# Kernel tuning notes

Measured on AMD Instinct MI355X. Metric: run time of the kernel, lower is better.

The kernel has to match this reference:

```python
import jax, jax.numpy as jnp
import numpy as np

B, L, D_IN, D_MODEL, D_OUT, N_LAYERS, N2 = 16, 2048, 512, 512, 512, 4, 32
Q_STEP = 1.0 / 64.0
LN_EPS = 1e-5


def setup_inputs() -> dict:
    key = jax.random.key(0)
    ks = jax.random.split(key, 12)
    H = D_MODEL
    x = jax.random.normal(ks[0], (B, D_IN, L), jnp.float32)
    # sigma-delta dense encoder / decoder weights (ANN-equivalent: dense + ReLU)
    W_enc = jax.random.normal(ks[1], (H, D_IN), jnp.float32) * (1.0 / np.sqrt(D_IN))
    W_dec = jax.random.normal(ks[2], (D_OUT, H), jnp.float32) * (1.0 / np.sqrt(H))
    # S4D kernel params, stacked over layers. S4D-Lin init.
    log_dt = (jax.random.uniform(ks[3], (N_LAYERS, H), jnp.float32)
              * (np.log(0.1) - np.log(0.001)) + np.log(0.001))
    log_A_real = jnp.full((N_LAYERS, H, N2), np.log(0.5), jnp.float32)
    A_imag = jnp.tile((np.pi * jnp.arange(N2, dtype=jnp.float32))[None, None, :],
                      (N_LAYERS, H, 1))
    C_re = jax.random.normal(ks[4], (N_LAYERS, H, N2), jnp.float32) * (0.5 ** 0.5)
    C_im = jax.random.normal(ks[5], (N_LAYERS, H, N2), jnp.float32) * (0.5 ** 0.5)
    D = jax.random.normal(ks[6], (N_LAYERS, H), jnp.float32)
    # output linear of each S4D block: 1x1 conv H -> 2H followed by GLU
    W_out = jax.random.normal(ks[7], (N_LAYERS, 2 * H, H), jnp.float32) * (1.0 / np.sqrt(H))
    b_out = jnp.zeros((N_LAYERS, 2 * H), jnp.float32)
    ln_g = jnp.ones((N_LAYERS, H), jnp.float32)
    ln_b = jnp.zeros((N_LAYERS, H), jnp.float32)
    return {"x": x, "W_enc": W_enc, "W_dec": W_dec, "log_dt": log_dt,
            "log_A_real": log_A_real, "A_imag": A_imag, "C_re": C_re,
            "C_im": C_im, "D": D, "W_out": W_out, "b_out": b_out,
            "ln_g": ln_g, "ln_b": ln_b}


def _quantize_ste(x, step):
    q = jnp.round(x / step) * step
    return x + jax.lax.stop_gradient(q - x)


def reference(x, W_enc, W_dec, log_dt, log_A_real, A_imag, C_re, C_im, D,
              W_out, b_out, ln_g, ln_b):
    # x: (B, d_input, L) channel-time layout (slayer convention)
    xq = _quantize_ste(x, Q_STEP)
    h = jax.nn.relu(jnp.einsum('bct,dc->bdt', xq, W_enc))  # encoder (B,H,L)
    Lx = h.shape[-1]
    t = jnp.arange(Lx)
    for i in range(N_LAYERS):
        # ---- S4D kernel (ZOH-style discretization) ----
        dt = jnp.exp(log_dt[i])[:, None]                 # (H,1)
        A = -jnp.exp(log_A_real[i]) + 1j * A_imag[i]     # (H,N)
        dtA = dt * A                                     # (H,N)
        Cc = (C_re[i] + 1j * C_im[i]) * jnp.expm1(dtA) / A
        vand = jnp.exp(dtA[:, :, None] * t)              # (H,N,L)
        K = 2.0 * jnp.einsum('hn,hnl->hl', Cc, vand).real  # (H,L)
        # ---- FFT convolution ----
        k_f = jnp.fft.rfft(K, n=2 * Lx)                  # (H, L+1)
        u_f = jnp.fft.rfft(h, n=2 * Lx)                  # (B,H,L+1)
        y = jnp.fft.irfft(u_f * k_f[None], n=2 * Lx)[..., :Lx]
        y = y + D[i][:, None] * h                        # skip connection
        y = jax.nn.gelu(y, approximate=False)
        # output linear: 1x1 conv H->2H + GLU over channel dim
        z = jnp.einsum('bht,dh->bdt', y, W_out[i]) + b_out[i][None, :, None]
        z = z[:, :D_MODEL] * jax.nn.sigmoid(z[:, D_MODEL:])
        # residual + post-norm (LayerNorm over channel dim)
        h = z + h
        mu = h.mean(axis=1, keepdims=True)
        var = h.var(axis=1, keepdims=True)
        h = (h - mu) / jnp.sqrt(var + LN_EPS) * ln_g[i][:, None] + ln_b[i][:, None]
    out = jax.nn.relu(jnp.einsum('bht,dh->bdt', h, W_dec))  # decoder (B,d_out,L)
    return out
```

## Files before the change

kernel.cpp:

```cpp
#include <hip/hip_runtime.h>
#include <cstdint>
#include <cstddef>

typedef __attribute__((ext_vector_type(8))) short short8;
typedef __attribute__((ext_vector_type(8))) _Float16 half8;
typedef __attribute__((ext_vector_type(4))) float floatx4;
typedef __attribute__((ext_vector_type(4))) int intx4;
typedef __attribute__((ext_vector_type(4))) unsigned short ushort4v;

__device__ __forceinline__ unsigned short f2h(float f) {
    union { _Float16 h; unsigned short u; } v;
    v.h = (_Float16)f;
    return v.u;
}
__device__ __forceinline__ float h2f(unsigned short u) {
    union { unsigned short u; _Float16 h; } v;
    v.u = u;
    return (float)v.h;
}
__device__ __forceinline__ float relu_keepnan(float v) {
    return v > 0.f ? v : (v == v ? 0.f : v);
}

__global__ __launch_bounds__(256) void k_cvt(
    const float* __restrict__ src, unsigned short* __restrict__ dst, int n) {
    int i = blockIdx.x * 256 + threadIdx.x;
    if (i < n) dst[i] = f2h(src[i]);
}

__global__ __launch_bounds__(256) void k_precompute(
    const float* __restrict__ ldt, const float* __restrict__ lar,
    const float* __restrict__ aim, const float* __restrict__ cre,
    const float* __restrict__ cim, float4* __restrict__ lwc,
    float2* __restrict__ wt) {
    int idx = blockIdx.x * 256 + threadIdx.x;
    int i = idx >> 14;
    int h = (idx >> 5) & 511;
    int n = idx & 31;
    float dt = expf(ldt[i * 512 + h]);
    float Are = -expf(lar[idx]);
    float Aim = aim[idx];
    float dre = dt * Are, dim = dt * Aim;
    float e = expf(dre);
    float wre = e * cosf(dim);
    float wim = e * sinf(dim);
    float emr = wre - 1.f, emi = wim;
    float inv = 1.f / (Are * Are + Aim * Aim);
    float fr = (emr * Are + emi * Aim) * inv;
    float fi = (emi * Are - emr * Aim) * inv;
    float cr = cre[idx], ci = cim[idx];
    float4 o;
    o.x = wre; o.y = wim;
    o.z = 2.f * (cr * fr - ci * fi);
    o.w = 2.f * (cr * fi + ci * fr);
    int oidx = (i * 32 + n) * 512 + h;
    lwc[oidx] = o;
    float ar = wre, ai = wim;
#pragma unroll
    for (int k = 0; k < 7; ++k) {
        float nr = ar * ar - ai * ai;
        float ni = 2.f * ar * ai;
        ar = nr; ai = ni;
    }
    wt[oidx] = make_float2(ar, ai);
}

__global__ __launch_bounds__(256) void k_quant_transpose(
    const float* __restrict__ x, unsigned short* __restrict__ xq, int b0) {
    __shared__ unsigned short tile[64][65];
    const int bg = b0 + blockIdx.z, bl = blockIdx.z;
    const int c0 = blockIdx.y * 64, t0 = blockIdx.x * 64;
    const int tid = threadIdx.x;
#pragma unroll
    for (int it = 0; it < 16; ++it) {
        int idx = it * 256 + tid;
        int r = idx >> 6, cc = idx & 63;
        float f = x[(size_t)(bg * 512 + c0 + r) * 2048 + t0 + cc];
        float q = rintf(f * 64.f) * 0.015625f;
        tile[r][cc] = f2h(q);
    }
    __syncthreads();
#pragma unroll
    for (int it = 0; it < 16; ++it) {
        int idx = it * 256 + tid;
        int r = idx >> 6, cc = idx & 63;
        xq[(size_t)(bl * 2048 + t0 + r) * 512 + c0 + cc] = tile[cc][r];
    }
}

__global__ __launch_bounds__(64) void k_build_wa(
    const float4* __restrict__ lwc, unsigned short* __restrict__ WA, int layer) {
    __shared__ unsigned short Ws[64 * 136];
    const int h = blockIdx.x, tid = threadIdx.x;
    if (tid < 32) {
        float4 v = lwc[((size_t)layer * 32 + tid) * 512 + h];
        float pr = 1.f, pi = 0.f;
        for (int m = 0; m < 128; ++m) {
            Ws[(2 * tid) * 136 + (127 - m)] = f2h(pr);
            Ws[(2 * tid + 1) * 136 + (127 - m)] = f2h(pi);
            float nr = pr * v.x - pi * v.y;
            float ni = pr * v.y + pi * v.x;
            pr = nr; pi = ni;
        }
    }
    __syncthreads();
#pragma unroll
    for (int it = 0; it < 16; ++it) {
        int idx = it * 64 + tid;
        int r = idx >> 4, c8 = idx & 15;
        *(intx4*)(WA + (size_t)h * 8192 + r * 128 + c8 * 8) =
            *(const intx4*)(Ws + r * 136 + c8 * 8);
    }
}

__global__ __launch_bounds__(256) void k_build_T(
    const float4* __restrict__ lwc, const float* __restrict__ Dp,
    unsigned short* __restrict__ TT, int layer) {
    __shared__ float Kvs[128];
    __shared__ unsigned short Mxs[128 * 64];
    __shared__ float wr_s[32], wi_s[32], cr_s[32], ci_s[32];
    const int h = blockIdx.x, tid = threadIdx.x;
    if (tid < 32) {
        float4 v = lwc[((size_t)layer * 32 + tid) * 512 + h];
        wr_s[tid] = v.x; wi_s[tid] = v.y; cr_s[tid] = v.z; ci_s[tid] = v.w;
    }
    __syncthreads();
    if (tid < 32) {
        const int n = tid;
        float wre = wr_s[n], wim = wi_s[n];
        float ar = cr_s[n], ai = ci_s[n];
        for (int m = 0; m <= 128; ++m) {
            if (m < 128) {
                float s = ar;
#pragma unroll
                for (int d = 16; d >= 1; d >>= 1) s += __shfl_xor(s, d, 64);
                if (n == 0) Kvs[m] = s;
            }
            if (m >= 1) {
                Mxs[(m - 1) * 64 + 2 * n] = f2h(ar);
                Mxs[(m - 1) * 64 + 2 * n + 1] = f2h(-ai);
            }
            float nr = ar * wre - ai * wim;
            float ni = ar * wim + ai * wre;
            ar = nr; ai = ni;
        }
    }
    __syncthreads();
    const float Dh = Dp[layer * 512 + h];
#pragma unroll
    for (int it = 0; it < 12; ++it) {
        int idx = it * 256 + tid;
        int t = idx / 24, c8 = idx % 24;
        short8 pack;
#pragma unroll
        for (int q = 0; q < 8; ++q) {
            int k = c8 * 8 + q;
            unsigned short us;
            if (k < 128) {
                float val = (k <= t) ? (Kvs[t - k] + (k == t ? Dh : 0.f)) : 0.f;
                us = f2h(val);
            } else {
                us = Mxs[t * 64 + (k - 128)];
            }
            pack[q] = (short)us;
        }
        *(short8*)(TT + (size_t)h * 24576 + t * 192 + c8 * 8) = pack;
    }
}

template <int MODE>
__global__ __launch_bounds__(256, 2) void k_gemm(
    const unsigned short* __restrict__ A, const unsigned short* __restrict__ Bm,
    float* __restrict__ of32, unsigned short* __restrict__ o16,
    unsigned short* __restrict__ ut, int J, int b0) {
    __shared__ __align__(16) unsigned short lds[2 * 128 * 72];
    unsigned short* Al = lds;
    unsigned short* Bl = lds + 128 * 72;
    const int tid = threadIdx.x;
    const int m0 = blockIdx.y * 128;
    const int j0 = blockIdx.x * 128;
    const int sub = tid & 7;
    const int row = tid >> 3;
    const unsigned short* Ag = A + (size_t)(m0 + row) * 512 + sub * 8;
    const unsigned short* Bg = Bm + (size_t)(j0 + row) * 512 + sub * 8;
    intx4 ra[4], rb[4];
#pragma unroll
    for (int i = 0; i < 4; ++i) {
        ra[i] = *(const intx4*)(Ag + (size_t)i * 32 * 512);
        rb[i] = *(const intx4*)(Bg + (size_t)i * 32 * 512);
    }
    const int lane = tid & 63;
    const int w = tid >> 6;
    const int wm = w & 1, wn = w >> 1;
    const int l15 = lane & 15, quad = lane >> 4;
    floatx4 acc[4][4] = {};
    for (int kt = 0; kt < 8; ++kt) {
#pragma unroll
        for (int i = 0; i < 4; ++i) {
            *(intx4*)(Al + (row + 32 * i) * 72 + sub * 8) = ra[i];
            *(intx4*)(Bl + (row + 32 * i) * 72 + sub * 8) = rb[i];
        }
        __syncthreads();
        if (kt < 7) {
#pragma unroll
            for (int i = 0; i < 4; ++i) {
                ra[i] = *(const intx4*)(Ag + (size_t)i * 32 * 512 + (kt + 1) * 64);
                rb[i] = *(const intx4*)(Bg + (size_t)i * 32 * 512 + (kt + 1) * 64);
            }
        }
#pragma unroll
        for (int ks = 0; ks < 2; ++ks) {
            half8 af[4], bfr[4];
#pragma unroll
            for (int mt = 0; mt < 4; ++mt)
                af[mt] = *(const half8*)(Al + (wm * 64 + mt * 16 + l15) * 72 + ks * 32 + quad * 8);
#pragma unroll
            for (int nt = 0; nt < 4; ++nt)
                bfr[nt] = *(const half8*)(Bl + (wn * 64 + nt * 16 + l15) * 72 + ks * 32 + quad * 8);
#pragma unroll
            for (int mt = 0; mt < 4; ++mt)
#pragma unroll
                for (int nt = 0; nt < 4; ++nt)
                    acc[mt][nt] = __builtin_amdgcn_mfma_f32_16x16x32_f16(
                        af[mt], bfr[nt], acc[mt][nt], 0, 0, 0);
        }
        __syncthreads();
    }
#pragma unroll
    for (int mt = 0; mt < 4; ++mt) {
#pragma unroll
        for (int nt = 0; nt < 4; ++nt) {
            const int dl = wm * 64 + mt * 16 + quad * 4;
            const int jl = wn * 64 + nt * 16 + l15;
            floatx4 v = acc[mt][nt];
#pragma unroll
            for (int r = 0; r < 4; ++r) v[r] = relu_keepnan(v[r]);
            if (MODE == 0) {
                ushort4v hv;
#pragma unroll
                for (int r = 0; r < 4; ++r) hv[r] = f2h(v[r]);
                *(ushort4v*)(o16 + (size_t)(j0 + jl) * 512 + m0 + dl) = hv;
#pragma unroll
                for (int r = 0; r < 4; ++r) lds[(dl + r) * 136 + jl] = hv[r];
            } else {
                const int j = j0 + jl;
                const int bl = j >> 11, t = j & 2047;
#pragma unroll
                for (int r = 0; r < 4; ++r)
                    of32[((size_t)((b0 + bl) * 512 + m0 + dl + r)) * 2048 + t] = v[r];
            }
        }
    }
    if (MODE == 0) {
        __syncthreads();
        const int drow = tid >> 1, hh = tid & 1;
        const unsigned short* srcp = lds + drow * 136 + hh * 64;
        unsigned short* dstp = ut + (size_t)(m0 + drow) * J + j0 + hh * 64;
#pragma unroll
        for (int q = 0; q < 8; ++q)
            *(intx4*)(dstp + q * 8) = *(const intx4*)(srcp + q * 8);
    }
}

__global__ __launch_bounds__(256, 4) void k_stateA(
    const unsigned short* __restrict__ WA, const unsigned short* __restrict__ ut,
    float* __restrict__ P, int J, int Rtot) {
    __shared__ __align__(16) unsigned short Aw[64 * 72];
    __shared__ __align__(16) unsigned short Bw[128 * 72];
    const int tid = threadIdx.x;
    const int h = blockIdx.y;
    const int r0 = blockIdx.x * 128;
    const int sub = tid & 7, row = tid >> 3;
    const unsigned short* Ag = WA + (size_t)h * 8192 + row * 128 + sub * 8;
    const unsigned short* Bg = ut + (size_t)h * J + (size_t)(r0 + row) * 128 + sub * 8;
    intx4 ra[2], rb[4];
    ra[0] = *(const intx4*)(Ag);
    ra[1] = *(const intx4*)(Ag + 32 * 128);
#pragma unroll
    for (int i = 0; i < 4; ++i) rb[i] = *(const intx4*)(Bg + i * 32 * 128);
    const int lane = tid & 63, w = tid >> 6;
    const int wm = w & 1, wn = w >> 1;
    const int l15 = lane & 15, quad = lane >> 4;
    floatx4 acc[2][4] = {};
    for (int kt = 0; kt < 2; ++kt) {
        *(intx4*)(Aw + row * 72 + sub * 8) = ra[0];
        *(intx4*)(Aw + (row + 32) * 72 + sub * 8) = ra[1];
#pragma unroll
        for (int i = 0; i < 4; ++i)
            *(intx4*)(Bw + (row + 32 * i) * 72 + sub * 8) = rb[i];
        __syncthreads();
        if (kt == 0) {
            ra[0] = *(const intx4*)(Ag + 64);
            ra[1] = *(const intx4*)(Ag + 32 * 128 + 64);
#pragma unroll
            for (int i = 0; i < 4; ++i) rb[i] = *(const intx4*)(Bg + i * 32 * 128 + 64);
        }
#pragma unroll
        for (int ks = 0; ks < 2; ++ks) {
            half8 af[2], bfr[4];
#pragma unroll
            for (int mt = 0; mt < 2; ++mt)
                af[mt] = *(const half8*)(Aw + (wm * 32 + mt * 16 + l15) * 72 + ks * 32 + quad * 8);
#pragma unroll
            for (int nt = 0; nt < 4; ++nt)
                bfr[nt] = *(const half8*)(Bw + (wn * 64 + nt * 16 + l15) * 72 + ks * 32 + quad * 8);
#pragma unroll
            for (int mt = 0; mt < 2; ++mt)
#pragma unroll
                for (int nt = 0; nt < 4; ++nt)
                    acc[mt][nt] = __builtin_amdgcn_mfma_f32_16x16x32_f16(
                        af[mt], bfr[nt], acc[mt][nt], 0, 0, 0);
        }
        __syncthreads();
    }
#pragma unroll
    for (int mt = 0; mt < 2; ++mt)
#pragma unroll
        for (int nt = 0; nt < 4; ++nt)
#pragma unroll
            for (int r = 0; r < 4; ++r)
                P[((size_t)h * 64 + wm * 32 + mt * 16 + quad * 4 + r) * Rtot +
                  r0 + wn * 64 + nt * 16 + l15] = acc[mt][nt][r];
}

__global__ __launch_bounds__(64) void k_comb(
    const float* __restrict__ P, const float2* __restrict__ wt,
    unsigned short* __restrict__ S0, int layer, int Rtot) {
    __shared__ float Ps[64][17];
    __shared__ unsigned short S0s[16][64];
    const int h = blockIdx.x, bl = blockIdx.y;
    const int tid = threadIdx.x;
#pragma unroll
    for (int it = 0; it < 4; ++it) {
        int idx = it * 64 + tid;
        int n2 = idx >> 2, pt = idx & 3;
        float4 v = *(const float4*)(P + ((size_t)h * 64 + n2) * Rtot + bl * 16 + pt * 4);
        Ps[n2][pt * 4 + 0] = v.x; Ps[n2][pt * 4 + 1] = v.y;
        Ps[n2][pt * 4 + 2] = v.z; Ps[n2][pt * 4 + 3] = v.w;
    }
    __syncthreads();
    if (tid < 32) {
        const int n = tid;
        float2 wv = wt[((size_t)layer * 32 + n) * 512 + h];
        float ar = 0.f, ai = 0.f;
        for (int g = 0; g < 16; ++g) {
            S0s[g][2 * n] = f2h(ar);
            S0s[g][2 * n + 1] = f2h(ai);
            float pr = Ps[2 * n][g], pi = Ps[2 * n + 1][g];
            float nr = fmaf(wv.x, ar, fmaf(-wv.y, ai, pr));
            float ni = fmaf(wv.x, ai, fmaf(wv.y, ar, pi));
            ar = nr; ai = ni;
        }
    }
    __syncthreads();
    const int g = tid >> 2, pt = tid & 3;
    unsigned short* dst = S0 + ((size_t)h * Rtot + bl * 16 + g) * 64 + pt * 16;
    *(intx4*)(dst) = *(const intx4*)(&S0s[g][pt * 16]);
    *(intx4*)(dst + 8) = *(const intx4*)(&S0s[g][pt * 16 + 8]);
}

__global__ __launch_bounds__(256, 2) void k_applyB(
    const unsigned short* __restrict__ TT, const unsigned short* __restrict__ ut,
    const unsigned short* __restrict__ S0, unsigned short* __restrict__ vt,
    int J, int Rtot) {
    __shared__ __align__(16) unsigned short lds[2 * 128 * 72];
    unsigned short* Al = lds;
    unsigned short* Bl = lds + 128 * 72;
    const int tid = threadIdx.x;
    const int h = blockIdx.y;
    const int r0 = blockIdx.x * 128;
    const int sub = tid & 7, row = tid >> 3;
    const unsigned short* Ag = TT + (size_t)h * 24576 + row * 192 + sub * 8;
    const unsigned short* Bu = ut + (size_t)h * J + (size_t)(r0 + row) * 128 + sub * 8;
    const unsigned short* Bs = S0 + ((size_t)h * Rtot + r0 + row) * 64 + sub * 8;
    intx4 ra[4], rb[4];
#pragma unroll
    for (int i = 0; i < 4; ++i) {
        ra[i] = *(const intx4*)(Ag + i * 32 * 192);
        rb[i] = *(const intx4*)(Bu + i * 32 * 128);
    }
    const int lane = tid & 63, w = tid >> 6;
    const int wm = w & 1, wn = w >> 1;
    const int l15 = lane & 15, quad = lane >> 4;
    floatx4 acc[4][4] = {};
    for (int kt = 0; kt < 3; ++kt) {
#pragma unroll
        for (int i = 0; i < 4; ++i) {
            *(intx4*)(Al + (row + 32 * i) * 72 + sub * 8) = ra[i];
            *(intx4*)(Bl + (row + 32 * i) * 72 + sub * 8) = rb[i];
        }
        __syncthreads();
        if (kt == 0) {
#pragma unroll
            for (int i = 0; i < 4; ++i) {
                ra[i] = *(const intx4*)(Ag + i * 32 * 192 + 64);
                rb[i] = *(const intx4*)(Bu + i * 32 * 128 + 64);
            }
        } else if (kt == 1) {
#pragma unroll
            for (int i = 0; i < 4; ++i) {
                ra[i] = *(const intx4*)(Ag + i * 32 * 192 + 128);
                rb[i] = *(const intx4*)(Bs + i * 32 * 64);
            }
        }
#pragma unroll
        for (int ks = 0; ks < 2; ++ks) {
            half8 af[4], bfr[4];
#pragma unroll
            for (int mt = 0; mt < 4; ++mt)
                af[mt] = *(const half8*)(Al + (wm * 64 + mt * 16 + l15) * 72 + ks * 32 + quad * 8);
#pragma unroll
            for (int nt = 0; nt < 4; ++nt)
                bfr[nt] = *(const half8*)(Bl + (wn * 64 + nt * 16 + l15) * 72 + ks * 32 + quad * 8);
#pragma unroll
            for (int mt = 0; mt < 4; ++mt)
#pragma unroll
                for (int nt = 0; nt < 4; ++nt)
                    acc[mt][nt] = __builtin_amdgcn_mfma_f32_16x16x32_f16(
                        af[mt], bfr[nt], acc[mt][nt], 0, 0, 0);
        }
        __syncthreads();
    }
#pragma unroll
    for (int mt = 0; mt < 4; ++mt)
#pragma unroll
        for (int nt = 0; nt < 4; ++nt) {
            const int tl = wm * 64 + mt * 16 + quad * 4;
            const int rl = wn * 64 + nt * 16 + l15;
            ushort4v pack;
#pragma unroll
            for (int r = 0; r < 4; ++r) {
                float y = acc[mt][nt][r];
                float ge = 0.5f * y * (1.f + erff(y * 0.70710678118654752f));
                pack[r] = f2h(ge);
            }
            *(ushort4v*)(lds + rl * 136 + tl) = pack;
        }
    __syncthreads();
    const int rl2 = tid >> 1, hh = tid & 1;
    const unsigned short* srcp = lds + rl2 * 136 + hh * 64;
    unsigned short* dstp = vt + (size_t)h * J + (size_t)(r0 + rl2) * 128 + hh * 64;
#pragma unroll
    for (int q = 0; q < 8; ++q)
        *(intx4*)(dstp + q * 8) = *(const intx4*)(srcp + q * 8);
}

__global__ __launch_bounds__(256, 2) void k_gemm_glu(
    const unsigned short* __restrict__ A,
    const unsigned short* __restrict__ Bt,
    const float* __restrict__ bias,
    unsigned short* __restrict__ g_out, int J) {
    __shared__ __align__(16) unsigned short lds[3 * 128 * 72];
    unsigned short* A1l = lds;
    unsigned short* A2l = lds + 9216;
    unsigned short* Bl  = lds + 18432;
    const int tid = threadIdx.x;
    const int m0 = blockIdx.y * 128;
    const int j0 = blockIdx.x * 128;
    const int sub = tid & 7;
    const int row = tid >> 3;
    const unsigned short* A1g = A + (size_t)(m0 + row) * 512 + sub * 8;
    const unsigned short* A2g = A1g + 512 * 512;
    const int chp = tid >> 3, jo = tid & 7;
    const unsigned short* Bg = Bt + (size_t)(2 * chp) * J + j0 + jo * 8;
    intx4 ra1[4], ra2[4], rb[4];
#pragma unroll
    for (int i = 0; i < 4; ++i) {
        ra1[i] = *(const intx4*)(A1g + (size_t)i * 32 * 512);
        ra2[i] = *(const intx4*)(A2g + (size_t)i * 32 * 512);
    }
    rb[0] = *(const intx4*)(Bg);
    rb[1] = *(const intx4*)(Bg + J);
    rb[2] = *(const intx4*)(Bg + 64);
    rb[3] = *(const intx4*)(Bg + J + 64);
    const int lane = tid & 63;
    const int w = tid >> 6;
    const int wm = w & 1, wn = w >> 1;
    const int l15 = lane & 15, quad = lane >> 4;
    const int colbase = (((chp >> 2) ^ jo) << 3) + (chp & 3) * 2;
    floatx4 ac1[4][4] = {}, ac2[4][4] = {};
    for (int kt = 0; kt < 8; ++kt) {
#pragma unroll
        for (int i = 0; i < 4; ++i) {
            *(intx4*)(A1l + (row + 32 * i) * 72 + sub * 8) = ra1[i];
            *(intx4*)(A2l + (row + 32 * i) * 72 + sub * 8) = ra2[i];
        }
        {
            unsigned int* B32 = (unsigned int*)Bl;
#pragma unroll
            for (int half = 0; half < 2; ++half) {
                const int jb = (jo + half * 8) * 8;
                intx4 e0 = rb[half * 2], e1 = rb[half * 2 + 1];
#pragma unroll
                for (int i = 0; i < 4; ++i) {
                    unsigned int ae = (unsigned int)e0[i], be = (unsigned int)e1[i];
                    unsigned int lo = (ae & 0xffffu) | (be << 16);
                    unsigned int hi = (ae >> 16) | (be & 0xffff0000u);
                    B32[((jb + 2 * i) * 72 + colbase) >> 1] = lo;
                    B32[((jb + 2 * i + 1) * 72 + colbase) >> 1] = hi;
                }
            }
        }
        __syncthreads();
        if (kt < 7) {
#pragma unroll
            for (int i = 0; i < 4; ++i) {
                ra1[i] = *(const intx4*)(A1g + (size_t)i * 32 * 512 + (kt + 1) * 64);
                ra2[i] = *(const intx4*)(A2g + (size_t)i * 32 * 512 + (kt + 1) * 64);
            }
            rb[0] = *(const intx4*)(Bg + (size_t)(kt + 1) * 64 * J);
            rb[1] = *(const intx4*)(Bg + (size_t)(kt + 1) * 64 * J + J);
            rb[2] = *(const intx4*)(Bg + (size_t)(kt + 1) * 64 * J + 64);
            rb[3] = *(const intx4*)(Bg + (size_t)(kt + 1) * 64 * J + J + 64);
        }
#pragma unroll
        for (int ks = 0; ks < 2; ++ks) {
            half8 af1[4], af2[4], bfr[4];
#pragma unroll
            for (int mt = 0; mt < 4; ++mt) {
                af1[mt] = *(const half8*)(A1l + (wm * 64 + mt * 16 + l15) * 72 + ks * 32 + quad * 8);
                af2[mt] = *(const half8*)(A2l + (wm * 64 + mt * 16 + l15) * 72 + ks * 32 + quad * 8);
            }
#pragma unroll
            for (int nt = 0; nt < 4; ++nt) {
                const int rr = wn * 64 + nt * 16 + l15;
                const int cb = (ks * 4 + quad) ^ ((rr >> 3) & 7);
                bfr[nt] = *(const half8*)(Bl + rr * 72 + cb * 8);
            }
#pragma unroll
            for (int mt = 0; mt < 4; ++mt)
#pragma unroll
                for (int nt = 0; nt < 4; ++nt) {
                    ac1[mt][nt] = __builtin_amdgcn_mfma_f32_16x16x32_f16(
                        af1[mt], bfr[nt], ac1[mt][nt], 0, 0, 0);
                    ac2[mt][nt] = __builtin_amdgcn_mfma_f32_16x16x32_f16(
                        af2[mt], bfr[nt], ac2[mt][nt], 0, 0, 0);
                }
        }
        __syncthreads();
    }
#pragma unroll
    for (int mt = 0; mt < 4; ++mt) {
#pragma unroll
        for (int nt = 0; nt < 4; ++nt) {
            const int dl = wm * 64 + mt * 16 + quad * 4;
            const int jl = wn * 64 + nt * 16 + l15;
            ushort4v p;
#pragma unroll
            for (int r = 0; r < 4; ++r) {
                float a = ac1[mt][nt][r] + bias[m0 + dl + r];
                float gg = ac2[mt][nt][r] + bias[512 + m0 + dl + r];
                p[r] = f2h(a / (1.f + expf(-gg)));
            }
            *(ushort4v*)(lds + jl * 136 + dl) = p;
        }
    }
    __syncthreads();
    const int r2 = tid >> 1, hh = tid & 1;
    const unsigned short* srcp = lds + r2 * 136 + hh * 64;
    unsigned short* dstp = g_out + (size_t)(j0 + r2) * 512 + m0 + hh * 64;
#pragma unroll
    for (int q = 0; q < 8; ++q)
        *(intx4*)(dstp + q * 8) = *(const intx4*)(srcp + q * 8);
}

__global__ __launch_bounds__(256, 4) void k_res_ln_t(
    const unsigned short* __restrict__ g, unsigned short* __restrict__ hf,
    unsigned short* __restrict__ ut, unsigned short* __restrict__ hb,
    const float* __restrict__ lng, const float* __restrict__ lnb,
    int layer, int J, int mode) {
    __shared__ unsigned short tile[64 * 40];
    const int tid = threadIdx.x;
    const int r = tid >> 3, sub = tid & 7;
    const int j0 = blockIdx.x * 32;
    const size_t j = (size_t)j0 + r;
    const unsigned short* gj = g + j * 512;
    unsigned short* hj = hf + j * 512;
    floatx4 v[16];
    float s1 = 0.f, s2 = 0.f;
#pragma unroll
    for (int k = 0; k < 16; ++k) {
        ushort4v gv = *(const ushort4v*)(gj + sub * 4 + k * 32);
        ushort4v hv = *(const ushort4v*)(hj + sub * 4 + k * 32);
        floatx4 vv;
#pragma unroll
        for (int i = 0; i < 4; ++i) vv[i] = h2f(gv[i]) + h2f(hv[i]);
        v[k] = vv;
        s1 += vv[0] + vv[1] + vv[2] + vv[3];
        s2 += vv[0] * vv[0] + vv[1] * vv[1] + vv[2] * vv[2] + vv[3] * vv[3];
    }
#pragma unroll
    for (int m = 4; m >= 1; m >>= 1) { s1 += __shfl_xor(s1, m, 64); s2 += __shfl_xor(s2, m, 64); }
    const float mu = s1 * (1.f / 512.f);
    const float var = s2 * (1.f / 512.f) - mu * mu;
    const float isd = 1.f / sqrtf(var + 1e-5f);
#pragma unroll
    for (int t = 0; t < 8; ++t) {
        if (mode == 1 && t) __syncthreads();
#pragma unroll
        for (int kk = 0; kk < 2; ++kk) {
            const int k = t * 2 + kk;
            const int cho = sub * 4 + k * 32;
            floatx4 gw = *(const floatx4*)(lng + layer * 512 + cho);
            floatx4 bw = *(const floatx4*)(lnb + layer * 512 + cho);
            ushort4v p;
#pragma unroll
            for (int i = 0; i < 4; ++i)
                p[i] = f2h((v[k][i] - mu) * isd * gw[i] + bw[i]);
            if (mode == 1) {
                *(ushort4v*)(hj + cho) = p;
                const int chl = kk * 32 + sub * 4;
#pragma unroll
                for (int i = 0; i < 4; ++i)
                    tile[(chl + i) * 40 + (r ^ ((((chl + i) >> 2) & 3) << 3))] = p[i];
            } else {
                *(ushort4v*)(hb + j * 512 + cho) = p;
            }
        }
        if (mode == 1) {
            __syncthreads();
            const int chrow = tid >> 2, part = tid & 3;
            const int pb = part ^ ((chrow >> 2) & 3);
            *(intx4*)(ut + (size_t)(t * 64 + chrow) * J + j0 + part * 8) =
                *(const intx4*)(tile + chrow * 40 + pb * 8);
        }
    }
}

extern "C" void kernel_launch(void* const* d_in, const int* in_sizes, int n_in,
                              void* d_out, int out_size, void* d_ws, size_t ws_size,
                              hipStream_t stream) {
    (void)in_sizes; (void)n_in; (void)out_size;
    const float* x      = (const float*)d_in[0];
    const float* W_enc  = (const float*)d_in[1];
    const float* W_dec  = (const float*)d_in[2];
    const float* log_dt = (const float*)d_in[3];
    const float* log_Ar = (const float*)d_in[4];
    const float* A_im   = (const float*)d_in[5];
    const float* C_re   = (const float*)d_in[6];
    const float* C_im   = (const float*)d_in[7];
    const float* Dp     = (const float*)d_in[8];
    const float* W_out  = (const float*)d_in[9];
    const float* b_out  = (const float*)d_in[10];
    const float* ln_g   = (const float*)d_in[11];
    const float* ln_b   = (const float*)d_in[12];

    int C = 16;
    while (C > 8 && (size_t)C * (9ull << 20) + (42ull << 20) > ws_size) C >>= 1;
    const size_t J = (size_t)C * 2048;
    const int Rtot = C * 16;

    char* ws = (char*)d_ws;
    size_t off = 0;
    auto alloc = [&](size_t bytes) { void* p = ws + off; off += (bytes + 255) & ~(size_t)255; return p; };
    float4*         lwc   = (float4*)alloc(4ull * 512 * 32 * 16);
    float2*         wt    = (float2*)alloc(4ull * 512 * 32 * 8);
    unsigned short* wencb = (unsigned short*)alloc(512 * 512 * 2);
    unsigned short* wdecb = (unsigned short*)alloc(512 * 512 * 2);
    unsigned short* woutb = (unsigned short*)alloc(4ull * 1024 * 512 * 2);
    unsigned short* WAb   = (unsigned short*)alloc(512ull * 64 * 128 * 2);
    unsigned short* TTb   = (unsigned short*)alloc(512ull * 128 * 192 * 2);
    unsigned short* ut    = (unsigned short*)alloc(512ull * J * 2);
    char*           scan  = (char*)alloc((size_t)C * (3ull << 20));
    unsigned short* hf    = (unsigned short*)alloc(J * 512 * 2);
    unsigned short* vt    = (unsigned short*)alloc(J * 512 * 2);
    unsigned short* g16   = (unsigned short*)scan;
    unsigned short* xq    = (unsigned short*)scan;
    unsigned short* hb    = vt;
    float*          P     = (float*)scan;
    unsigned short* S0u   = (unsigned short*)(scan + (size_t)C * (2ull << 20));

    k_precompute<<<256, 256, 0, stream>>>(log_dt, log_Ar, A_im, C_re, C_im, lwc, wt);
    k_cvt<<<1024, 256, 0, stream>>>(W_enc, wencb, 512 * 512);
    k_cvt<<<1024, 256, 0, stream>>>(W_dec, wdecb, 512 * 512);
    k_cvt<<<8192, 256, 0, stream>>>(W_out, woutb, 4 * 1024 * 512);
    for (int b0 = 0; b0 < 16; b0 += C) {
        k_quant_transpose<<<dim3(32, 8, C), 256, 0, stream>>>(x, xq, b0);
        k_gemm<0><<<dim3(C * 16, 4), 256, 0, stream>>>(wencb, xq, nullptr, hf, ut, (int)J, 0);
        for (int i = 0; i < 4; ++i) {
            k_build_wa<<<512, 64, 0, stream>>>(lwc, WAb, i);
            k_build_T<<<512, 256, 0, stream>>>(lwc, Dp, TTb, i);
            k_stateA<<<dim3(Rtot / 128, 512), 256, 0, stream>>>(WAb, ut, P, (int)J, Rtot);
            k_comb<<<dim3(512, C), 64, 0, stream>>>(P, wt, S0u, i, Rtot);
            k_applyB<<<dim3(Rtot / 128, 512), 256, 0, stream>>>(TTb, ut, S0u, vt, (int)J, Rtot);
            k_gemm_glu<<<dim3(C * 16, 4), 256, 0, stream>>>(
                woutb + (size_t)i * 1024 * 512, vt, b_out + (size_t)i * 1024, g16, (int)J);
            k_res_ln_t<<<(int)(J / 32), 256, 0, stream>>>(
                g16, hf, ut, hb, ln_g, ln_b, i, (int)J, (i == 3) ? 2 : 1);
        }
        k_gemm<2><<<dim3(C * 16, 4), 256, 0, stream>>>(wdecb, hb, (float*)d_out, nullptr, nullptr, (int)J, b0);
    }
}
```

Before: 928.8 us.

## Fuse chunk-state GEMM with intra-block state combine, raise occupancy bounds

Merges the per-chunk state projection GEMM and the sequential complex state-combine kernel into one kernel. Partial states now stay in LDS instead of round-tripping through a global fp32 buffer, and one kernel launch per layer is removed. Launch-bound minimum blocks for k_gemm and k_applyB are also raised from 2 to 3 to push occupancy, which risks register spills. The combine now runs per 16-chunk group inside each 128-chunk tile, with 256 threads doing the serial recurrences.

```diff
diff --git a/kernel.cpp b/kernel.cpp
--- a/kernel.cpp
+++ b/kernel.cpp
@@ -169,7 +169,7 @@
 }
 
 template <int MODE>
-__global__ __launch_bounds__(256, 2) void k_gemm(
+__global__ __launch_bounds__(256, 3) void k_gemm(
     const unsigned short* __restrict__ A, const unsigned short* __restrict__ Bm,
     float* __restrict__ of32, unsigned short* __restrict__ o16,
     unsigned short* __restrict__ ut, int J, int b0) {
@@ -262,11 +262,14 @@
     }
 }
 
-__global__ __launch_bounds__(256, 4) void k_stateA(
+__global__ __launch_bounds__(256, 4) void k_stateA_comb(
     const unsigned short* __restrict__ WA, const unsigned short* __restrict__ ut,
-    float* __restrict__ P, int J, int Rtot) {
-    __shared__ __align__(16) unsigned short Aw[64 * 72];
-    __shared__ __align__(16) unsigned short Bw[128 * 72];
+    const float2* __restrict__ wt, unsigned short* __restrict__ S0,
+    int layer, int J, int Rtot) {
+    __shared__ __align__(16) char smem[64 * 131 * 4];
+    unsigned short* Aw = (unsigned short*)smem;
+    unsigned short* Bw = (unsigned short*)(smem + 64 * 72 * 2);
+    float* Ps = (float*)smem;
     const int tid = threadIdx.x;
     const int h = blockIdx.y;
     const int r0 = blockIdx.x * 128;
@@ -319,47 +322,25 @@
         for (int nt = 0; nt < 4; ++nt)
 #pragma unroll
             for (int r = 0; r < 4; ++r)
-                P[((size_t)h * 64 + wm * 32 + mt * 16 + quad * 4 + r) * Rtot +
-                  r0 + wn * 64 + nt * 16 + l15] = acc[mt][nt][r];
-}
-
-__global__ __launch_bounds__(64) void k_comb(
-    const float* __restrict__ P, const float2* __restrict__ wt,
-    unsigned short* __restrict__ S0, int layer, int Rtot) {
-    __shared__ float Ps[64][17];
-    __shared__ unsigned short S0s[16][64];
-    const int h = blockIdx.x, bl = blockIdx.y;
-    const int tid = threadIdx.x;
-#pragma unroll
-    for (int it = 0; it < 4; ++it) {
-        int idx = it * 64 + tid;
-        int n2 = idx >> 2, pt = idx & 3;
-        float4 v = *(const float4*)(P + ((size_t)h * 64 + n2) * Rtot + bl * 16 + pt * 4);
-        Ps[n2][pt * 4 + 0] = v.x; Ps[n2][pt * 4 + 1] = v.y;
-        Ps[n2][pt * 4 + 2] = v.z; Ps[n2][pt * 4 + 3] = v.w;
-    }
+                Ps[(wm * 32 + mt * 16 + quad * 4 + r) * 131 +
+                   wn * 64 + nt * 16 + l15] = acc[mt][nt][r];
     __syncthreads();
-    if (tid < 32) {
-        const int n = tid;
-        float2 wv = wt[((size_t)layer * 32 + n) * 512 + h];
-        float ar = 0.f, ai = 0.f;
-        for (int g = 0; g < 16; ++g) {
-            S0s[g][2 * n] = f2h(ar);
-            S0s[g][2 * n + 1] = f2h(ai);
-            float pr = Ps[2 * n][g], pi = Ps[2 * n + 1][g];
-            float nr = fmaf(wv.x, ar, fmaf(-wv.y, ai, pr));
-            float ni = fmaf(wv.x, ai, fmaf(wv.y, ar, pi));
-            ar = nr; ai = ni;
-        }
-    }
-    __syncthreads();
-    const int g = tid >> 2, pt = tid & 3;
-    unsigned short* dst = S0 + ((size_t)h * Rtot + bl * 16 + g) * 64 + pt * 16;
-    *(intx4*)(dst) = *(const intx4*)(&S0s[g][pt * 16]);
-    *(intx4*)(dst + 8) = *(const intx4*)(&S0s[g][pt * 16 + 8]);
-}
-
-__global__ __launch_bounds__(256, 2) void k_applyB(
+    const int n = tid & 31, bl = tid >> 5;
+    const float2 wv = wt[((size_t)layer * 32 + n) * 512 + h];
+    unsigned int* S0w = (unsigned int*)(S0 + ((size_t)h * Rtot + r0 + bl * 16) * 64) + n;
+    float ar = 0.f, ai = 0.f;
+#pragma unroll
+    for (int g = 0; g < 16; ++g) {
+        S0w[g * 32] = (unsigned int)f2h(ar) | ((unsigned int)f2h(ai) << 16);
+        float pr = Ps[(2 * n) * 131 + bl * 16 + g];
+        float pi = Ps[(2 * n + 1) * 131 + bl * 16 + g];
+        float nr = fmaf(wv.x, ar, fmaf(-wv.y, ai, pr));
+        float ni = fmaf(wv.x, ai, fmaf(wv.y, ar, pi));
+        ar = nr; ai = ni;
+    }
+}
+
+__global__ __launch_bounds__(256, 3) void k_applyB(
     const unsigned short* __restrict__ TT, const unsigned short* __restrict__ ut,
     const unsigned short* __restrict__ S0, unsigned short* __restrict__ vt,
     int J, int Rtot) {
@@ -667,7 +648,6 @@
     unsigned short* g16   = (unsigned short*)scan;
     unsigned short* xq    = (unsigned short*)scan;
     unsigned short* hb    = vt;
-    float*          P     = (float*)scan;
     unsigned short* S0u   = (unsigned short*)(scan + (size_t)C * (2ull << 20));
 
     k_precompute<<<256, 256, 0, stream>>>(log_dt, log_Ar, A_im, C_re, C_im, lwc, wt);
@@ -680,8 +660,8 @@
         for (int i = 0; i < 4; ++i) {
             k_build_wa<<<512, 64, 0, stream>>>(lwc, WAb, i);
             k_build_T<<<512, 256, 0, stream>>>(lwc, Dp, TTb, i);
-            k_stateA<<<dim3(Rtot / 128, 512), 256, 0, stream>>>(WAb, ut, P, (int)J, Rtot);
-            k_comb<<<dim3(512, C), 64, 0, stream>>>(P, wt, S0u, i, Rtot);
+            k_stateA_comb<<<dim3(Rtot / 128, 512), 256, 0, stream>>>(
+                WAb, ut, wt, S0u, i, (int)J, Rtot);
             k_applyB<<<dim3(Rtot / 128, 512), 256, 0, stream>>>(TTb, ut, S0u, vt, (int)J, Rtot);
             k_gemm_glu<<<dim3(C * 16, 4), 256, 0, stream>>>(
                 woutb + (size_t)i * 1024 * 512, vt, b_out + (size_t)i * 1024, g16, (int)J);
```

Result: faster. 874.0 us (-5.9%).
